# Performance work log

Measured on AMD Instinct MI355X. Metric: run time of the kernel, lower is better.

The kernel has to match this reference:

```python
import jax, jax.numpy as jnp
import numpy as np

HIDDEN = 1024
HEADS = 16


def rotate_half(x):
    x1, x2 = jnp.split(x, 2, axis=-1)
    return jnp.concatenate((-x2, x1), axis=-1)


def rope_tables(seq_len, dim):
    inv_freq = 1.0 / 10000 ** (jnp.arange(0, dim, 2, dtype=jnp.float32) / dim)
    t = jnp.arange(seq_len, dtype=jnp.float32)
    freqs = jnp.outer(t, inv_freq)
    emb = jnp.concatenate((freqs, freqs), axis=-1)  # [S, dim]
    return jnp.cos(emb), jnp.sin(emb)


def setup_inputs() -> dict:
    key = jax.random.key(0)
    ks = jax.random.split(key, 10)
    B, S, D = 2, 2048, HIDDEN
    scale = 1.0 / np.sqrt(D)
    inp = {
        "inputs": jax.random.normal(ks[0], (B, S, D), jnp.float32),
        "context": jax.random.normal(ks[1], (B, S, D), jnp.float32),
        "Wq": jax.random.normal(ks[2], (D, D), jnp.float32) * scale,
        "bq": jnp.zeros((D,), jnp.float32),
        "Wk": jax.random.normal(ks[3], (D, D), jnp.float32) * scale,
        "bk": jnp.zeros((D,), jnp.float32),
        "Wv": jax.random.normal(ks[4], (D, D), jnp.float32) * scale,
        "bv": jnp.zeros((D,), jnp.float32),
        "Wo": jax.random.normal(ks[5], (D, D), jnp.float32) * scale,
        "bo": jnp.zeros((D,), jnp.float32),
    }
    return inp


def reference(inputs, context, Wq, bq, Wk, bk, Wv, bv, Wo, bo):
    B, S, D = inputs.shape
    H = HEADS
    hd = D // H

    q = inputs @ Wq + bq          # [B,S,D]
    k = context @ Wk + bk
    v = context @ Wv + bv

    # RoPE applied over the FULL hidden dim, pre-head-split (faithful to source).
    cos, sin = rope_tables(S, D)  # [S,D]
    # source indexes [0] after broadcasting with [1,1,S,D] tables -> effectively same values
    q = q * cos + rotate_half(q) * sin
    k = k * cos + rotate_half(k) * sin

    q = q.reshape(B, S, H, hd)
    k = k.reshape(B, S, H, hd)
    v = v.reshape(B, S, H, hd)

    # Faithful: NO transpose before attention; matmul contracts last dims of
    # q [B,S,H,hd] with k^T [B,S,hd,H] -> scores [B,S,H,H]
    scores = jnp.einsum('bshd,btd->bsht', q, jnp.zeros((1, 1, 1))) if False else None
    scores = jnp.matmul(q, jnp.swapaxes(k, -2, -1)) / jnp.sqrt(jnp.float32(hd))  # [B,S,H,H]
    attn = jax.nn.softmax(scores, axis=-1)
    ctx = jnp.matmul(attn, v)     # [B,S,H,hd]

    # source: transpose(0,2,1,3) then reshape back to (B,S,D)
    ctx = ctx.transpose(0, 2, 1, 3).reshape(B, S, D)
    out = ctx @ Wo + bo
    return out, attn
```

## Files before the change

### kernel.cpp

```cpp
#include <hip/hip_runtime.h>
#include <hip/hip_bf16.h>
#include <cstdint>

typedef __attribute__((ext_vector_type(8))) short short8;
typedef __attribute__((ext_vector_type(4))) float f32x4;
typedef __attribute__((ext_vector_type(4))) float float4v;
typedef __attribute__((ext_vector_type(4))) unsigned short us4;

#define HD 1024
#define SEQ 2048

__device__ __forceinline__ unsigned short f2bf(float f) {
  uint32_t u = __builtin_bit_cast(uint32_t, f);
  return (unsigned short)((u + 0x7FFFu + ((u >> 16) & 1u)) >> 16);
}
__device__ __forceinline__ float bf2f(unsigned short s) {
  return __builtin_bit_cast(float, (uint32_t)s << 16);
}

__device__ __forceinline__ void gload16(const unsigned short* g, unsigned short* l) {
  __builtin_amdgcn_global_load_lds(
      (const __attribute__((address_space(1))) void*)g,
      (__attribute__((address_space(3))) void*)l, 16, 0, 0);
}

__global__ __launch_bounds__(256) void prep(
    const float* __restrict__ X, const float* __restrict__ Y,
    const float* __restrict__ w0, const float* __restrict__ w1,
    const float* __restrict__ w2, const float* __restrict__ w3,
    unsigned short* __restrict__ Xh, unsigned short* __restrict__ Yh,
    unsigned short* __restrict__ wt) {
  __shared__ float tile[32][33];
  int bx = blockIdx.x;
  int tid = threadIdx.x;
  if (bx < 4096) {
    const float* src = (bx >= 2048) ? Y : X;
    unsigned short* oh = (bx >= 2048) ? Yh : Xh;
    int i0 = (bx & 2047) * 512 + tid;
#pragma unroll
    for (int r = 0; r < 2; ++r) {
      int i = i0 + r * 256;
      float4v v = ((const float4v*)src)[i];
      us4 h;
#pragma unroll
      for (int j = 0; j < 4; ++j) h[j] = f2bf(v[j]);
      ((us4*)oh)[i] = h;
    }
  } else {
    int t = bx - 4096;
    int z = t >> 10;
    int rem = t & 1023;
    int bxx = rem & 31, byy = rem >> 5;
    const float* in = (z == 0) ? w0 : (z == 1) ? w1 : (z == 2) ? w2 : w3;
    unsigned short* oh = wt + (size_t)z * 1024 * 1024;
    int tx = tid & 31, ty = tid >> 5;
    int x = bxx * 32 + tx;
    int y0 = byy * 32;
    for (int i = ty; i < 32; i += 8)
      tile[i][tx] = in[(size_t)(y0 + i) * HD + x];
    __syncthreads();
    int x2 = y0 + tx;
    int y2 = bxx * 32;
    for (int i = ty; i < 32; i += 8)
      oh[(size_t)(y2 + i) * HD + x2] = f2bf(tile[tx][i]);
  }
}

__global__ __launch_bounds__(256, 3) void gemm_qkv(
    const unsigned short* __restrict__ Ih, const unsigned short* __restrict__ Ch,
    const unsigned short* __restrict__ wt,
    const float* __restrict__ bq, const float* __restrict__ bk, const float* __restrict__ bv,
    unsigned short* __restrict__ qo, unsigned short* __restrict__ ko,
    unsigned short* __restrict__ vo) {
  __shared__ __align__(16) unsigned short lds[2][128][64];
  const int K = HD, N = HD;
  const size_t P = (size_t)1024 * 1024;
  int z  = blockIdx.z;
  const unsigned short* Ah = z ? Ch : Ih;
  const unsigned short* Bth = wt + (size_t)z * P;
  const float* bias = (z == 0) ? bq : (z == 1) ? bk : bv;
  unsigned short* C = (z == 0) ? qo : (z == 1) ? ko : vo;

  int m0 = blockIdx.x * 128;
  int n0 = blockIdx.y * 128;
  int tid  = threadIdx.x;
  int lane = tid & 63;
  int w    = tid >> 6;
  int quad = lane >> 4;
  int l16  = lane & 15;
  int wm = (w >> 1) * 64;
  int wn = (w & 1) * 64;

  int ro = lane >> 3;
  int sl = lane & 7;
  int ge = sl ^ (ro >> 1);
  int go = ge ^ 4;
  const unsigned short* spA_e = Ah  + (size_t)(m0 + ro) * K + ge * 8;
  const unsigned short* spA_o = Ah  + (size_t)(m0 + ro) * K + go * 8;
  const unsigned short* spB_e = Bth + (size_t)(n0 + ro) * K + ge * 8;
  const unsigned short* spB_o = Bth + (size_t)(n0 + ro) * K + go * 8;

  f32x4 acc[4][4];
#pragma unroll
  for (int t = 0; t < 4; ++t)
#pragma unroll
    for (int u = 0; u < 4; ++u) acc[t][u] = (f32x4){0.f, 0.f, 0.f, 0.f};

  for (int k0 = 0; k0 < K; k0 += 64) {
    __syncthreads();
#pragma unroll
    for (int i = 0; i < 4; ++i) {
      int seg = w + i * 4;
      const unsigned short* pa = (seg & 1) ? spA_o : spA_e;
      const unsigned short* pb = (seg & 1) ? spB_o : spB_e;
      gload16(pa + (size_t)seg * 8 * K + k0, &lds[0][seg * 8][0]);
      gload16(pb + (size_t)seg * 8 * K + k0, &lds[1][seg * 8][0]);
    }
    __syncthreads();

#pragma unroll
    for (int j = 0; j < 2; ++j) {
      int sl8 = (((j << 2) | quad) ^ (l16 >> 1)) * 8;
      short8 ah[4], bh[4];
#pragma unroll
      for (int t = 0; t < 4; ++t)
        ah[t] = *(const short8*)&lds[0][wm + t * 16 + l16][sl8];
#pragma unroll
      for (int u = 0; u < 4; ++u)
        bh[u] = *(const short8*)&lds[1][wn + u * 16 + l16][sl8];
#pragma unroll
      for (int t = 0; t < 4; ++t)
#pragma unroll
        for (int u = 0; u < 4; ++u)
          acc[t][u] = __builtin_amdgcn_mfma_f32_16x16x32_bf16(ah[t], bh[u], acc[t][u], 0, 0, 0);
    }
  }

#pragma unroll
  for (int t = 0; t < 4; ++t) {
    int row = m0 + wm + t * 16 + quad * 4;
#pragma unroll
    for (int u = 0; u < 4; ++u) {
      int col = n0 + wn + u * 16 + l16;
      float bvv = bias[col];
#pragma unroll
      for (int i = 0; i < 4; ++i)
        C[(size_t)(row + i) * N + col] = f2bf(acc[t][u][i] + bvv);
    }
  }
}

__global__ __launch_bounds__(256, 3) void gemm_o(
    const unsigned short* __restrict__ Ah, const unsigned short* __restrict__ Bth,
    const float* __restrict__ bias, float* __restrict__ C) {
  __shared__ __align__(16) unsigned short ldsA[128][64];
  __shared__ __align__(16) unsigned short ldsB[64][64];
  const int K = HD, N = HD;
  int m0 = blockIdx.x * 128;
  int n0 = blockIdx.y * 64;
  int tid  = threadIdx.x;
  int lane = tid & 63;
  int w    = tid >> 6;
  int quad = lane >> 4;
  int l16  = lane & 15;
  int wm = (w >> 1) * 64;
  int wn = (w & 1) * 32;

  int ro = lane >> 3;
  int sl = lane & 7;
  int ge = sl ^ (ro >> 1);
  int go = ge ^ 4;
  const unsigned short* spA_e = Ah  + (size_t)(m0 + ro) * K + ge * 8;
  const unsigned short* spA_o = Ah  + (size_t)(m0 + ro) * K + go * 8;
  const unsigned short* spB_e = Bth + (size_t)(n0 + ro) * K + ge * 8;
  const unsigned short* spB_o = Bth + (size_t)(n0 + ro) * K + go * 8;

  f32x4 acc[4][2];
#pragma unroll
  for (int t = 0; t < 4; ++t)
#pragma unroll
    for (int u = 0; u < 2; ++u) acc[t][u] = (f32x4){0.f, 0.f, 0.f, 0.f};

  for (int k0 = 0; k0 < K; k0 += 64) {
    __syncthreads();
#pragma unroll
    for (int i = 0; i < 4; ++i) {
      int seg = w + i * 4;
      const unsigned short* pa = (seg & 1) ? spA_o : spA_e;
      gload16(pa + (size_t)seg * 8 * K + k0, &ldsA[seg * 8][0]);
    }
#pragma unroll
    for (int i = 0; i < 2; ++i) {
      int seg = w + i * 4;
      const unsigned short* pb = (seg & 1) ? spB_o : spB_e;
      gload16(pb + (size_t)seg * 8 * K + k0, &ldsB[seg * 8][0]);
    }
    __syncthreads();

#pragma unroll
    for (int j = 0; j < 2; ++j) {
      int sl8 = (((j << 2) | quad) ^ (l16 >> 1)) * 8;
      short8 ah[4], bh[2];
#pragma unroll
      for (int t = 0; t < 4; ++t)
        ah[t] = *(const short8*)&ldsA[wm + t * 16 + l16][sl8];
#pragma unroll
      for (int u = 0; u < 2; ++u)
        bh[u] = *(const short8*)&ldsB[wn + u * 16 + l16][sl8];
#pragma unroll
      for (int t = 0; t < 4; ++t)
#pragma unroll
        for (int u = 0; u < 2; ++u)
          acc[t][u] = __builtin_amdgcn_mfma_f32_16x16x32_bf16(ah[t], bh[u], acc[t][u], 0, 0, 0);
    }
  }

#pragma unroll
  for (int t = 0; t < 4; ++t) {
    int row = m0 + wm + t * 16 + quad * 4;
#pragma unroll
    for (int u = 0; u < 2; ++u) {
      int col = n0 + wn + u * 16 + l16;
      float bvv = bias[col];
#pragma unroll
      for (int i = 0; i < 4; ++i)
        C[(size_t)(row + i) * N + col] = acc[t][u][i] + bvv;
    }
  }
}

__global__ __launch_bounds__(256) void attn_rope_k(
    const unsigned short* __restrict__ q, const unsigned short* __restrict__ kk,
    const unsigned short* __restrict__ v,
    float* __restrict__ attn_out, unsigned short* __restrict__ ctx_h) {
  __shared__ float qs[16][68], ks[16][68], vs[16][68], as[16][17];
  int m = blockIdx.x;
  int tid = threadIdx.x;
  int s = m & (SEQ - 1);
  size_t base4 = (size_t)m * (HD / 4);
  {
    int h = tid >> 4, dd = (tid & 15) * 4;
    us4 qv = ((const us4*)q)[base4 + tid];
    us4 kv = ((const us4*)kk)[base4 + tid];
    us4 vv = ((const us4*)v)[base4 + tid];
#pragma unroll
    for (int j = 0; j < 4; ++j) {
      qs[h][dd + j] = bf2f(qv[j]);
      ks[h][dd + j] = bf2f(kv[j]);
      vs[h][dd + j] = bf2f(vv[j]);
    }
  }
  __syncthreads();
#pragma unroll
  for (int d = tid; d < 512; d += 256) {
    float f = exp2f(-(float)d * 0.025952563241307517f);
    float rev = (float)s * (f * 0.15915494309189535f);
    rev -= floorf(rev);
    float sv = __builtin_amdgcn_sinf(rev);
    float cv = __builtin_amdgcn_cosf(rev);
    int h1 = d >> 6, dd = d & 63, h2 = h1 + 8;
    float q1 = qs[h1][dd], q2 = qs[h2][dd];
    qs[h1][dd] = q1 * cv - q2 * sv;
    qs[h2][dd] = q2 * cv + q1 * sv;
    float k1 = ks[h1][dd], k2 = ks[h2][dd];
    ks[h1][dd] = k1 * cv - k2 * sv;
    ks[h2][dd] = k2 * cv + k1 * sv;
  }
  __syncthreads();
  int h = tid >> 4, t = tid & 15;
  float sc = 0.f;
#pragma unroll
  for (int d = 0; d < 64; ++d) sc = fmaf(qs[h][d], ks[t][d], sc);
  sc *= 0.125f;
  float mx = sc;
  mx = fmaxf(mx, __shfl_xor(mx, 1));
  mx = fmaxf(mx, __shfl_xor(mx, 2));
  mx = fmaxf(mx, __shfl_xor(mx, 4));
  mx = fmaxf(mx, __shfl_xor(mx, 8));
  float e = expf(sc - mx);
  float sum = e;
  sum += __shfl_xor(sum, 1);
  sum += __shfl_xor(sum, 2);
  sum += __shfl_xor(sum, 4);
  sum += __shfl_xor(sum, 8);
  float a = e / sum;
  attn_out[(size_t)m * 256 + tid] = a;
  as[h][t] = a;
  __syncthreads();
  int b = m >> 11;
  for (int j = tid; j < 1024; j += 256) {
    int h2 = j >> 6, d = j & 63;
    float c = 0.f;
#pragma unroll
    for (int t2 = 0; t2 < 16; ++t2) c = fmaf(as[h2][t2], vs[t2][d], c);
    int row = b * SEQ + h2 * 128 + (s >> 4);
    int col = (s & 15) * 64 + d;
    ctx_h[(size_t)row * HD + col] = f2bf(c);
  }
}

extern "C" void kernel_launch(void* const* d_in, const int* in_sizes, int n_in,
                              void* d_out, int out_size, void* d_ws, size_t ws_size,
                              hipStream_t stream) {
  const float* inputs  = (const float*)d_in[0];
  const float* context = (const float*)d_in[1];
  const float* Wq = (const float*)d_in[2];
  const float* bq = (const float*)d_in[3];
  const float* Wk = (const float*)d_in[4];
  const float* bk = (const float*)d_in[5];
  const float* Wv = (const float*)d_in[6];
  const float* bv = (const float*)d_in[7];
  const float* Wo = (const float*)d_in[8];
  const float* bo = (const float*)d_in[9];

  float* out  = (float*)d_out;
  float* attn = out + (size_t)4096 * 1024;

  const size_t MB = 1ull << 20;
  char* wsb = (char*)d_ws;
  unsigned short* q  = (unsigned short*)(wsb + 0 * MB);
  unsigned short* k  = (unsigned short*)(wsb + 8 * MB);
  unsigned short* v  = (unsigned short*)(wsb + 16 * MB);
  unsigned short* wt = (unsigned short*)(wsb + 24 * MB);
  unsigned short* Ih = (unsigned short*)(wsb + 32 * MB);
  unsigned short* Ch = (unsigned short*)(wsb + 40 * MB);
  unsigned short* ctxh = Ih;

  prep<<<8192, 256, 0, stream>>>(inputs, context, Wq, Wk, Wv, Wo, Ih, Ch, wt);

  gemm_qkv<<<dim3(32, 8, 3), 256, 0, stream>>>(Ih, Ch, wt, bq, bk, bv, q, k, v);

  attn_rope_k<<<4096, 256, 0, stream>>>(q, k, v, attn, ctxh);

  const size_t P = (size_t)1024 * 1024;
  gemm_o<<<dim3(32, 16), 256, 0, stream>>>(ctxh, wt + 3 * P, bo, out);
}
```

Baseline: 166.5 us.

## Restructure attention kernel to one wave per token with MFMA scores

The attention/RoPE kernel now assigns one 64-lane wave per sequence position, four per block, instead of a full 256-thread block per position. RoPE is applied in registers using cross-lane shuffles. The 16x16 head score matrix is computed with bf16 MFMA instructions, and V is loaded asynchronously into LDS via global_load_lds. This removes block-wide syncs and most LDS traffic. The trade-off is that q and k are rounded to bf16 before the score product, which lowers precision of the attention output.

New measurement: 161.7 us. 1.03x faster.

```diff
diff --git a/kernel.cpp b/kernel.cpp
--- a/kernel.cpp
+++ b/kernel.cpp
@@ -233,70 +233,135 @@
     const unsigned short* __restrict__ q, const unsigned short* __restrict__ kk,
     const unsigned short* __restrict__ v,
     float* __restrict__ attn_out, unsigned short* __restrict__ ctx_h) {
-  __shared__ float qs[16][68], ks[16][68], vs[16][68], as[16][17];
-  int m = blockIdx.x;
+  __shared__ __align__(16) unsigned short vs[4][16][64];
   int tid = threadIdx.x;
+  int lane = tid & 63;
+  int w = tid >> 6;
+  int m = blockIdx.x * 4 + w;
   int s = m & (SEQ - 1);
-  size_t base4 = (size_t)m * (HD / 4);
+  int b = m >> 11;
+  int l16 = lane & 15;
+  int quad = lane >> 4;
+
   {
-    int h = tid >> 4, dd = (tid & 15) * 4;
-    us4 qv = ((const us4*)q)[base4 + tid];
-    us4 kv = ((const us4*)kk)[base4 + tid];
-    us4 vv = ((const us4*)v)[base4 + tid];
-#pragma unroll
-    for (int j = 0; j < 4; ++j) {
-      qs[h][dd + j] = bf2f(qv[j]);
-      ks[h][dd + j] = bf2f(kv[j]);
-      vs[h][dd + j] = bf2f(vv[j]);
-    }
-  }
-  __syncthreads();
-#pragma unroll
-  for (int d = tid; d < 512; d += 256) {
-    float f = exp2f(-(float)d * 0.025952563241307517f);
-    float rev = (float)s * (f * 0.15915494309189535f);
-    rev -= floorf(rev);
-    float sv = __builtin_amdgcn_sinf(rev);
-    float cv = __builtin_amdgcn_cosf(rev);
-    int h1 = d >> 6, dd = d & 63, h2 = h1 + 8;
-    float q1 = qs[h1][dd], q2 = qs[h2][dd];
-    qs[h1][dd] = q1 * cv - q2 * sv;
-    qs[h2][dd] = q2 * cv + q1 * sv;
-    float k1 = ks[h1][dd], k2 = ks[h2][dd];
-    ks[h1][dd] = k1 * cv - k2 * sv;
-    ks[h2][dd] = k2 * cv + k1 * sv;
-  }
-  __syncthreads();
-  int h = tid >> 4, t = tid & 15;
-  float sc = 0.f;
-#pragma unroll
-  for (int d = 0; d < 64; ++d) sc = fmaf(qs[h][d], ks[t][d], sc);
-  sc *= 0.125f;
-  float mx = sc;
-  mx = fmaxf(mx, __shfl_xor(mx, 1));
-  mx = fmaxf(mx, __shfl_xor(mx, 2));
-  mx = fmaxf(mx, __shfl_xor(mx, 4));
-  mx = fmaxf(mx, __shfl_xor(mx, 8));
-  float e = expf(sc - mx);
-  float sum = e;
-  sum += __shfl_xor(sum, 1);
-  sum += __shfl_xor(sum, 2);
-  sum += __shfl_xor(sum, 4);
-  sum += __shfl_xor(sum, 8);
-  float a = e / sum;
-  attn_out[(size_t)m * 256 + tid] = a;
-  as[h][t] = a;
-  __syncthreads();
-  int b = m >> 11;
-  for (int j = tid; j < 1024; j += 256) {
-    int h2 = j >> 6, d = j & 63;
-    float c = 0.f;
-#pragma unroll
-    for (int t2 = 0; t2 < 16; ++t2) c = fmaf(as[h2][t2], vs[t2][d], c);
-    int row = b * SEQ + h2 * 128 + (s >> 4);
-    int col = (s & 15) * 64 + d;
-    ctx_h[(size_t)row * HD + col] = f2bf(c);
-  }
+    unsigned short* dst = &vs[w][0][0];
+    const unsigned short* src = v + (size_t)m * HD;
+    gload16(src + lane * 8, dst);
+    gload16(src + 512 + lane * 8, dst + 512);
+  }
+
+  const unsigned short* qrow = q + (size_t)m * HD + l16 * 64 + quad * 8;
+  const unsigned short* krow = kk + (size_t)m * HD + l16 * 64 + quad * 8;
+  float qf[2][8], kf[2][8];
+#pragma unroll
+  for (int j = 0; j < 2; ++j) {
+    short8 qv = *(const short8*)(qrow + j * 32);
+    short8 kv = *(const short8*)(krow + j * 32);
+#pragma unroll
+    for (int e = 0; e < 8; ++e) {
+      qf[j][e] = bf2f((unsigned short)qv[e]);
+      kf[j][e] = bf2f((unsigned short)kv[e]);
+    }
+  }
+
+  const float C = 0.025952563241307517f;
+  const float I2PI = 0.15915494309189535f;
+  float fs = (float)s;
+  int pbase = (l16 & 7) * 64 + quad * 8;
+  bool hi = (l16 & 8) != 0;
+#pragma unroll
+  for (int j = 0; j < 2; ++j) {
+#pragma unroll
+    for (int e = 0; e < 8; ++e) {
+      int p = pbase + j * 32 + e;
+      float f = exp2f(-(float)p * C);
+      float rev = fs * f * I2PI;
+      rev -= floorf(rev);
+      float sv = __builtin_amdgcn_sinf(rev);
+      float cv = __builtin_amdgcn_cosf(rev);
+      float pq = __shfl_xor(qf[j][e], 8);
+      float pk = __shfl_xor(kf[j][e], 8);
+      float sg = hi ? sv : -sv;
+      qf[j][e] = qf[j][e] * cv + pq * sg;
+      kf[j][e] = kf[j][e] * cv + pk * sg;
+    }
+  }
+
+  short8 qh[2], kh[2];
+#pragma unroll
+  for (int j = 0; j < 2; ++j)
+#pragma unroll
+    for (int e = 0; e < 8; ++e) {
+      qh[j][e] = (short)f2bf(qf[j][e]);
+      kh[j][e] = (short)f2bf(kf[j][e]);
+    }
+
+  f32x4 acc = (f32x4){0.f, 0.f, 0.f, 0.f};
+  acc = __builtin_amdgcn_mfma_f32_16x16x32_bf16(kh[0], qh[0], acc, 0, 0, 0);
+  acc = __builtin_amdgcn_mfma_f32_16x16x32_bf16(kh[1], qh[1], acc, 0, 0, 0);
+
+  float sc[4];
+#pragma unroll
+  for (int i = 0; i < 4; ++i) sc[i] = acc[i] * 0.125f;
+  float mx = fmaxf(fmaxf(sc[0], sc[1]), fmaxf(sc[2], sc[3]));
+  mx = fmaxf(mx, __shfl_xor(mx, 16));
+  mx = fmaxf(mx, __shfl_xor(mx, 32));
+  float ee[4];
+  float sum = 0.f;
+#pragma unroll
+  for (int i = 0; i < 4; ++i) { ee[i] = expf(sc[i] - mx); sum += ee[i]; }
+  sum += __shfl_xor(sum, 16);
+  sum += __shfl_xor(sum, 32);
+  float inv = 1.0f / sum;
+  f32x4 av;
+#pragma unroll
+  for (int i = 0; i < 4; ++i) av[i] = ee[i] * inv;
+
+  *(f32x4*)(attn_out + (size_t)m * 256 + l16 * 16 + quad * 4) = av;
+
+  float sh[4][4];
+#pragma unroll
+  for (int i = 0; i < 4; ++i) {
+    sh[0][i] = av[i];
+    sh[1][i] = __shfl_xor(av[i], 16);
+    sh[2][i] = __shfl_xor(av[i], 32);
+    sh[3][i] = __shfl_xor(sh[1][i], 32);
+  }
+
+  asm volatile("s_waitcnt vmcnt(0)" ::: "memory");
+  float c[16];
+#pragma unroll
+  for (int d = 0; d < 16; ++d) c[d] = 0.f;
+  const unsigned short(*vw)[64] = vs[w];
+  int d0 = quad * 16;
+#pragma unroll
+  for (int qq = 0; qq < 4; ++qq) {
+    int tb = ((quad ^ qq) << 2);
+#pragma unroll
+    for (int i = 0; i < 4; ++i) {
+      int t = tb + i;
+      float aval = sh[qq][i];
+      short8 v0 = *(const short8*)&vw[t][d0];
+      short8 v1 = *(const short8*)&vw[t][d0 + 8];
+#pragma unroll
+      for (int d = 0; d < 8; ++d) {
+        c[d]     = fmaf(aval, bf2f((unsigned short)v0[d]), c[d]);
+        c[8 + d] = fmaf(aval, bf2f((unsigned short)v1[d]), c[8 + d]);
+      }
+    }
+  }
+
+  int row = b * SEQ + l16 * 128 + (s >> 4);
+  int col = (s & 15) * 64 + d0;
+  unsigned short* cp = ctx_h + (size_t)row * HD + col;
+  short8 o0, o1;
+#pragma unroll
+  for (int d = 0; d < 8; ++d) {
+    o0[d] = (short)f2bf(c[d]);
+    o1[d] = (short)f2bf(c[8 + d]);
+  }
+  *(short8*)cp = o0;
+  *((short8*)(cp + 8)) = o1;
 }
 
 extern "C" void kernel_launch(void* const* d_in, const int* in_sizes, int n_in,
@@ -330,7 +395,7 @@
 
   gemm_qkv<<<dim3(32, 8, 3), 256, 0, stream>>>(Ih, Ch, wt, bq, bk, bv, q, k, v);
 
-  attn_rope_k<<<4096, 256, 0, stream>>>(q, k, v, attn, ctxh);
+  attn_rope_k<<<1024, 256, 0, stream>>>(q, k, v, attn, ctxh);
 
   const size_t P = (size_t)1024 * 1024;
   gemm_o<<<dim3(32, 16), 256, 0, stream>>>(ctxh, wt + 3 * P, bo, out);
```
